# Kernel tuning notes

Measured on AMD Instinct MI355X. Metric: run time of the kernel, lower is better.

Reference implementation:

```python
import jax, jax.numpy as jnp
import numpy as np

C_CURV = 0.01   # manifold curvature c
EPS = 1e-7
KH = KW = 3
PAD = 1
STRIDE = 1


def log0(y):
    # Poincare-ball log map at origin: artanh(sqrt(c)||y||) * y / (sqrt(c)||y||)
    sqc = jnp.sqrt(jnp.asarray(C_CURV, y.dtype))
    n = jnp.maximum(jnp.linalg.norm(y, axis=-1, keepdims=True), EPS)
    return jnp.arctanh(jnp.clip(sqc * n, 0.0, 1.0 - 1e-6)) * y / (sqc * n)


def exp0(v):
    # Poincare-ball exp map at origin: tanh(sqrt(c)||v||) * v / (sqrt(c)||v||)
    sqc = jnp.sqrt(jnp.asarray(C_CURV, v.dtype))
    n = jnp.maximum(jnp.linalg.norm(v, axis=-1, keepdims=True), EPS)
    return jnp.tanh(sqc * n) * v / (sqc * n)


def setup_inputs() -> dict:
    key = jax.random.key(0)
    k1, k2, k3 = jax.random.split(key, 3)
    x = jax.random.uniform(k1, (4, 32, 256, 256), dtype=jnp.float32)  # points in ball (c=0.01 -> radius 10)
    Wk = jax.random.normal(k2, (KH * KW, 32, 32), dtype=jnp.float32) * 0.05  # [K, C_out, C_in]
    bias = jax.random.normal(k3, (32,), dtype=jnp.float32) * 0.01
    return {"x": x, "Wk": Wk, "bias": bias}


def reference(x, Wk, bias):
    B, Cin, H, W = x.shape
    Hout = (H + 2 * PAD - KH) // STRIDE + 1
    Wout = (W + 2 * PAD - KW) // STRIDE + 1
    xp = jnp.pad(x, ((0, 0), (0, 0), (PAD, PAD), (PAD, PAD)))
    # unfold: one slice per kernel position (i,j), matching F.unfold's (C_in, K, L) layout
    patches = jnp.stack(
        [xp[:, :, i:i + Hout * STRIDE:STRIDE, j:j + Wout * STRIDE:STRIDE]
         for i in range(KH) for j in range(KW)], axis=0)      # [K, B, Cin, Hout, Wout]
    u = log0(jnp.moveaxis(patches, 2, -1))                    # [K, B, Hout, Wout, Cin] tangent vectors
    # PVFC (mobius matvec = exp0(W @ log0(x))) followed by log0 cancels the exp0:
    # log0(PVFC_k(x)) = W_k @ log0(x). Aggregate (sum over k) fused into the einsum.
    v = jnp.einsum('kbhwc,koc->bhwo', u, Wk)                  # [B, Hout, Wout, Cout]
    v = jax.nn.relu(v + bias)
    out = exp0(v)                                             # back to manifold
    return jnp.transpose(out, (0, 3, 1, 2))                   # [B, Cout, Hout, Wout]
```

## Files before the change

### kernel.cpp

```cpp
#include <hip/hip_runtime.h>
#include <math.h>


#define TW 32
#define TH 8
#define HW_ 34
#define NPIX 340
#define CIN 32
#define COUT 32
#define U_BYTES 21760
#define W_ROWS 288

typedef __attribute__((ext_vector_type(8))) short bf16x8;
typedef __attribute__((ext_vector_type(4))) float f32x4;

__device__ inline unsigned short f2bf(float f) {
    unsigned int u = __builtin_bit_cast(unsigned int, f);
    unsigned int r = (u + 0x7FFFu + ((u >> 16) & 1u)) >> 16;
    return (unsigned short)r;
}

__global__ __launch_bounds__(256, 4) void pvconv_kernel(
    const float* __restrict__ x, const float* __restrict__ Wk,
    const float* __restrict__ bias, float* __restrict__ out)
{
    __shared__ __align__(16) unsigned char smem[U_BYTES + W_ROWS * 64];
    unsigned char* u8 = smem;
    unsigned char* w8 = smem + U_BYTES;
    float*         v  = (float*)smem;

    const int t  = threadIdx.x;
    const int bx = blockIdx.x, by = blockIdx.y, b = blockIdx.z;
    const int x0 = bx * TW, y0 = by * TH;

    for (int f = t; f < W_ROWS * 4; f += 256) {
        int r = f >> 2, j = f & 3;
        const float4* src = (const float4*)(Wk + r * 32 + j * 8);
        float4 a = src[0], c = src[1];
        unsigned int pk[4];
        pk[0] = (unsigned int)f2bf(a.x) | ((unsigned int)f2bf(a.y) << 16);
        pk[1] = (unsigned int)f2bf(a.z) | ((unsigned int)f2bf(a.w) << 16);
        pk[2] = (unsigned int)f2bf(c.x) | ((unsigned int)f2bf(c.y) << 16);
        pk[3] = (unsigned int)f2bf(c.z) | ((unsigned int)f2bf(c.w) << 16);
        int sw = j ^ ((r >> 1) & 3);
        *(uint4*)(w8 + r * 64 + sw * 16) = *(uint4*)pk;
    }

    for (int p = t; p < NPIX; p += 256) {
        int py = p / HW_, px = p - py * HW_;
        int gy = y0 - 1 + py, gx = x0 - 1 + px;
        float vv[CIN];
        if ((unsigned)gy < 256u && (unsigned)gx < 256u) {
            const float* xp = x + (size_t)b * CIN * 65536 + gy * 256 + gx;
            #pragma unroll
            for (int c = 0; c < CIN; ++c) vv[c] = xp[(size_t)c * 65536];
        } else {
            #pragma unroll
            for (int c = 0; c < CIN; ++c) vv[c] = 0.f;
        }
        float ss = 0.f;
        #pragma unroll
        for (int c = 0; c < CIN; ++c) ss = fmaf(vv[c], vv[c], ss);
        float n = fmaxf(sqrtf(ss), 1e-7f);
        float z = fminf(0.1f * n, 1.f - 1e-6f);
        float at = 0.5f * __logf((1.f + z) / (1.f - z));
        float s = at / (0.1f * n);
        int swb = (p >> 1) & 3;
        uint4* row = (uint4*)(u8 + p * 64);
        #pragma unroll
        for (int j = 0; j < 4; ++j) {
            unsigned int pk[4];
            #pragma unroll
            for (int w = 0; w < 4; ++w)
                pk[w] = (unsigned int)f2bf(vv[j * 8 + 2 * w] * s)
                      | ((unsigned int)f2bf(vv[j * 8 + 2 * w + 1] * s) << 16);
            row[j ^ swb] = *(uint4*)pk;
        }
    }
    __syncthreads();

    const int wv = t >> 6, lane = t & 63;
    const int m = lane & 15, quad = lane >> 4;

    f32x4 acc[2][4];
    #pragma unroll
    for (int n = 0; n < 2; ++n)
        #pragma unroll
        for (int mt = 0; mt < 4; ++mt) acc[n][mt] = (f32x4)0.f;

    int apix[4];
    #pragma unroll
    for (int mt = 0; mt < 4; ++mt) {
        int pb = wv * 64 + mt * 16;
        apix[mt] = (pb >> 5) * HW_ + (pb & 31) + m;
    }

    #pragma unroll
    for (int tap = 0; tap < 9; ++tap) {
        const int dy = tap / 3, dx = tap - dy * 3;
        const int hoff = dy * HW_ + dx;
        int r0 = tap * 32 + m;
        int swB = quad ^ ((r0 >> 1) & 3);
        bf16x8 bf0 = *(const bf16x8*)(w8 + r0 * 64 + swB * 16);
        bf16x8 bf1 = *(const bf16x8*)(w8 + (r0 + 16) * 64 + swB * 16);
        #pragma unroll
        for (int mt = 0; mt < 4; ++mt) {
            int hp = apix[mt] + hoff;
            bf16x8 af = *(const bf16x8*)(u8 + hp * 64 + ((quad ^ ((hp >> 1) & 3)) << 4));
            acc[0][mt] = __builtin_amdgcn_mfma_f32_16x16x32_bf16(af, bf0, acc[0][mt], 0, 0, 0);
            acc[1][mt] = __builtin_amdgcn_mfma_f32_16x16x32_bf16(af, bf1, acc[1][mt], 0, 0, 0);
        }
    }

    const float bia0 = bias[m], bia1 = bias[16 + m];
    __syncthreads();

    #pragma unroll
    for (int n = 0; n < 2; ++n)
        #pragma unroll
        for (int mt = 0; mt < 4; ++mt)
            #pragma unroll
            for (int r = 0; r < 4; ++r) {
                int pix = wv * 64 + mt * 16 + quad * 4 + r;
                float val = acc[n][mt][r] + (n ? bia1 : bia0);
                v[pix * 36 + n * 16 + m] = fmaxf(val, 0.f);
            }
    __syncthreads();

    {
        float q[COUT];
        const float4* vp = (const float4*)(smem + (size_t)t * 144);
        #pragma unroll
        for (int j = 0; j < 8; ++j) {
            float4 c4 = vp[j];
            q[4 * j] = c4.x; q[4 * j + 1] = c4.y; q[4 * j + 2] = c4.z; q[4 * j + 3] = c4.w;
        }
        float ss = 0.f;
        #pragma unroll
        for (int o = 0; o < COUT; ++o) ss = fmaf(q[o], q[o], ss);
        float n = fmaxf(sqrtf(ss), 1e-7f);
        float a = 0.1f * n;
        float e = __expf(-2.f * a);
        float s = (1.f - e) / ((1.f + e) * a);
        const int px = t & 31, py = t >> 5;
        const size_t base = (size_t)b * COUT * 65536 + (size_t)(y0 + py) * 256 + (x0 + px);
        #pragma unroll
        for (int o = 0; o < COUT; ++o)
            out[base + (size_t)o * 65536] = s * q[o];
    }
}

extern "C" void kernel_launch(void* const* d_in, const int* in_sizes, int n_in,
                              void* d_out, int out_size, void* d_ws, size_t ws_size,
                              hipStream_t stream) {
    const float* x    = (const float*)d_in[0];
    const float* Wk   = (const float*)d_in[1];
    const float* bias = (const float*)d_in[2];
    float* out = (float*)d_out;

    dim3 grid(256 / TW, 256 / TH, 4);
    dim3 block(256);
    pvconv_kernel<<<grid, block, 0, stream>>>(x, Wk, bias, out);
}
```

Before: 98.00 us.

## Prepack bf16 weights, vectorize halo loads, use 512-thread blocks with bf16 staging

```diff
diff --git a/kernel.cpp b/kernel.cpp
--- a/kernel.cpp
+++ b/kernel.cpp
@@ -8,145 +8,146 @@
 #define NPIX 340
 #define CIN 32
 #define COUT 32
-#define U_BYTES 21760
-#define W_ROWS 288
 
 typedef __attribute__((ext_vector_type(8))) short bf16x8;
 typedef __attribute__((ext_vector_type(4))) float f32x4;
 
 __device__ inline unsigned short f2bf(float f) {
     unsigned int u = __builtin_bit_cast(unsigned int, f);
-    unsigned int r = (u + 0x7FFFu + ((u >> 16) & 1u)) >> 16;
-    return (unsigned short)r;
+    return (unsigned short)((u + 0x7FFFu + ((u >> 16) & 1u)) >> 16);
+}
+__device__ inline unsigned int pk2(float a, float b) {
+    return (unsigned int)f2bf(a) | ((unsigned int)f2bf(b) << 16);
 }
 
-__global__ __launch_bounds__(256, 4) void pvconv_kernel(
-    const float* __restrict__ x, const float* __restrict__ Wk,
+__global__ __launch_bounds__(256) void wprep_kernel(
+    const float* __restrict__ Wk, unsigned short* __restrict__ wsW)
+{
+    int i = blockIdx.x * 256 + threadIdx.x;
+    if (i < 9 * 32 * 32) wsW[i] = f2bf(Wk[i]);
+}
+
+__global__ __launch_bounds__(512, 8) void pvconv_kernel(
+    const float* __restrict__ x, const unsigned short* __restrict__ wsW,
     const float* __restrict__ bias, float* __restrict__ out)
 {
-    __shared__ __align__(16) unsigned char smem[U_BYTES + W_ROWS * 64];
+    __shared__ __align__(16) unsigned char smem[NPIX * 64];
     unsigned char* u8 = smem;
-    unsigned char* w8 = smem + U_BYTES;
-    float*         v  = (float*)smem;
 
     const int t  = threadIdx.x;
-    const int bx = blockIdx.x, by = blockIdx.y, b = blockIdx.z;
-    const int x0 = bx * TW, y0 = by * TH;
+    const int x0 = blockIdx.x * TW, y0 = blockIdx.y * TH, b = blockIdx.z;
 
-    for (int f = t; f < W_ROWS * 4; f += 256) {
-        int r = f >> 2, j = f & 3;
-        const float4* src = (const float4*)(Wk + r * 32 + j * 8);
-        float4 a = src[0], c = src[1];
-        unsigned int pk[4];
-        pk[0] = (unsigned int)f2bf(a.x) | ((unsigned int)f2bf(a.y) << 16);
-        pk[1] = (unsigned int)f2bf(a.z) | ((unsigned int)f2bf(a.w) << 16);
-        pk[2] = (unsigned int)f2bf(c.x) | ((unsigned int)f2bf(c.y) << 16);
-        pk[3] = (unsigned int)f2bf(c.z) | ((unsigned int)f2bf(c.w) << 16);
-        int sw = j ^ ((r >> 1) & 3);
-        *(uint4*)(w8 + r * 64 + sw * 16) = *(uint4*)pk;
-    }
-
-    for (int p = t; p < NPIX; p += 256) {
-        int py = p / HW_, px = p - py * HW_;
-        int gy = y0 - 1 + py, gx = x0 - 1 + px;
-        float vv[CIN];
-        if ((unsigned)gy < 256u && (unsigned)gx < 256u) {
-            const float* xp = x + (size_t)b * CIN * 65536 + gy * 256 + gx;
+    if (t < 400) {
+        const int hy = t / 40, rem = t - hy * 40, j = rem >> 2, cq = rem & 3;
+        const int gy = y0 - 1 + hy;
+        const int gxb = x0 - 4 + 4 * j;
+        const bool ok = ((unsigned)gy < 256u) && !(j == 0 && x0 == 0)
+                                              && !(j == 9 && x0 == 224);
+        float vv[4][8];
+        if (ok) {
+            const float* xp = x + (size_t)(b * CIN + cq * 8) * 65536 + gy * 256 + gxb;
             #pragma unroll
-            for (int c = 0; c < CIN; ++c) vv[c] = xp[(size_t)c * 65536];
+            for (int cc = 0; cc < 8; ++cc) {
+                float4 f4 = *(const float4*)(xp + (size_t)cc * 65536);
+                vv[0][cc] = f4.x; vv[1][cc] = f4.y; vv[2][cc] = f4.z; vv[3][cc] = f4.w;
+            }
         } else {
             #pragma unroll
-            for (int c = 0; c < CIN; ++c) vv[c] = 0.f;
+            for (int i = 0; i < 4; ++i)
+                #pragma unroll
+                for (int cc = 0; cc < 8; ++cc) vv[i][cc] = 0.f;
         }
-        float ss = 0.f;
+        float s4[4];
         #pragma unroll
-        for (int c = 0; c < CIN; ++c) ss = fmaf(vv[c], vv[c], ss);
-        float n = fmaxf(sqrtf(ss), 1e-7f);
-        float z = fminf(0.1f * n, 1.f - 1e-6f);
-        float at = 0.5f * __logf((1.f + z) / (1.f - z));
-        float s = at / (0.1f * n);
-        int swb = (p >> 1) & 3;
-        uint4* row = (uint4*)(u8 + p * 64);
+        for (int i = 0; i < 4; ++i) {
+            float ss = 0.f;
+            #pragma unroll
+            for (int cc = 0; cc < 8; ++cc) ss = fmaf(vv[i][cc], vv[i][cc], ss);
+            ss += __shfl_xor(ss, 1);
+            ss += __shfl_xor(ss, 2);
+            float n = fmaxf(sqrtf(ss), 1e-7f);
+            float z = fminf(0.1f * n, 1.f - 1e-6f);
+            float at = 0.5f * __logf((1.f + z) / (1.f - z));
+            s4[i] = at / (0.1f * n);
+        }
+        const int i0 = (j == 0) ? 3 : 0, i1 = (j == 9) ? 0 : 3;
         #pragma unroll
-        for (int j = 0; j < 4; ++j) {
-            unsigned int pk[4];
+        for (int i = 0; i < 4; ++i) {
+            if (i < i0 || i > i1) continue;
+            int p = hy * 34 + 4 * j - 3 + i;
+            unsigned int pkk[4];
             #pragma unroll
             for (int w = 0; w < 4; ++w)
-                pk[w] = (unsigned int)f2bf(vv[j * 8 + 2 * w] * s)
-                      | ((unsigned int)f2bf(vv[j * 8 + 2 * w + 1] * s) << 16);
-            row[j ^ swb] = *(uint4*)pk;
+                pkk[w] = pk2(vv[i][2 * w] * s4[i], vv[i][2 * w + 1] * s4[i]);
+            *(uint4*)(u8 + p * 64 + ((cq ^ ((p >> 1) & 3)) << 4)) = *(uint4*)pkk;
         }
     }
     __syncthreads();
 
-    const int wv = t >> 6, lane = t & 63;
-    const int m = lane & 15, quad = lane >> 4;
+    const int wv = t >> 6, lane = t & 63, m = lane & 15, quad = lane >> 4;
+    const float bia0 = bias[m], bia1 = bias[16 + m];
 
-    f32x4 acc[2][4];
+    f32x4 acc[2][2];
     #pragma unroll
     for (int n = 0; n < 2; ++n)
         #pragma unroll
-        for (int mt = 0; mt < 4; ++mt) acc[n][mt] = (f32x4)0.f;
+        for (int mt = 0; mt < 2; ++mt) acc[n][mt] = (f32x4)0.f;
 
-    int apix[4];
-    #pragma unroll
-    for (int mt = 0; mt < 4; ++mt) {
-        int pb = wv * 64 + mt * 16;
-        apix[mt] = (pb >> 5) * HW_ + (pb & 31) + m;
-    }
-
+    const int pb0 = wv * 34 + m;
     #pragma unroll
     for (int tap = 0; tap < 9; ++tap) {
         const int dy = tap / 3, dx = tap - dy * 3;
-        const int hoff = dy * HW_ + dx;
-        int r0 = tap * 32 + m;
-        int swB = quad ^ ((r0 >> 1) & 3);
-        bf16x8 bf0 = *(const bf16x8*)(w8 + r0 * 64 + swB * 16);
-        bf16x8 bf1 = *(const bf16x8*)(w8 + (r0 + 16) * 64 + swB * 16);
+        const unsigned short* wrow = wsW + (tap * 32 + m) * 32 + quad * 8;
+        bf16x8 B0 = *(const bf16x8*)wrow;
+        bf16x8 B1 = *(const bf16x8*)(wrow + 512);
         #pragma unroll
-        for (int mt = 0; mt < 4; ++mt) {
-            int hp = apix[mt] + hoff;
-            bf16x8 af = *(const bf16x8*)(u8 + hp * 64 + ((quad ^ ((hp >> 1) & 3)) << 4));
-            acc[0][mt] = __builtin_amdgcn_mfma_f32_16x16x32_bf16(af, bf0, acc[0][mt], 0, 0, 0);
-            acc[1][mt] = __builtin_amdgcn_mfma_f32_16x16x32_bf16(af, bf1, acc[1][mt], 0, 0, 0);
+        for (int mt = 0; mt < 2; ++mt) {
+            int p = pb0 + mt * 16 + dy * 34 + dx;
+            bf16x8 A = *(const bf16x8*)(u8 + p * 64 + ((quad ^ ((p >> 1) & 3)) << 4));
+            acc[0][mt] = __builtin_amdgcn_mfma_f32_16x16x32_bf16(A, B0, acc[0][mt], 0, 0, 0);
+            acc[1][mt] = __builtin_amdgcn_mfma_f32_16x16x32_bf16(A, B1, acc[1][mt], 0, 0, 0);
         }
     }
-
-    const float bia0 = bias[m], bia1 = bias[16 + m];
     __syncthreads();
 
+    unsigned short* vb = (unsigned short*)smem;
     #pragma unroll
     for (int n = 0; n < 2; ++n)
         #pragma unroll
-        for (int mt = 0; mt < 4; ++mt)
+        for (int mt = 0; mt < 2; ++mt)
             #pragma unroll
             for (int r = 0; r < 4; ++r) {
-                int pix = wv * 64 + mt * 16 + quad * 4 + r;
+                int P = wv * 32 + mt * 16 + quad * 4 + r;
                 float val = acc[n][mt][r] + (n ? bia1 : bia0);
-                v[pix * 36 + n * 16 + m] = fmaxf(val, 0.f);
+                vb[P * 40 + n * 16 + m] = f2bf(fmaxf(val, 0.f));
             }
     __syncthreads();
 
     {
-        float q[COUT];
-        const float4* vp = (const float4*)(smem + (size_t)t * 144);
+        const int pix = t >> 1, h = t & 1;
+        const unsigned short* vp = (const unsigned short*)smem + pix * 40 + h * 16;
+        uint4 q0 = *(const uint4*)vp;
+        uint4 q1 = *(const uint4*)(vp + 8);
+        unsigned int wds[8] = {q0.x, q0.y, q0.z, q0.w, q1.x, q1.y, q1.z, q1.w};
+        float qf[16];
         #pragma unroll
-        for (int j = 0; j < 8; ++j) {
-            float4 c4 = vp[j];
-            q[4 * j] = c4.x; q[4 * j + 1] = c4.y; q[4 * j + 2] = c4.z; q[4 * j + 3] = c4.w;
+        for (int k = 0; k < 8; ++k) {
+            qf[2 * k]     = __builtin_bit_cast(float, wds[k] << 16);
+            qf[2 * k + 1] = __builtin_bit_cast(float, wds[k] & 0xFFFF0000u);
         }
         float ss = 0.f;
         #pragma unroll
-        for (int o = 0; o < COUT; ++o) ss = fmaf(q[o], q[o], ss);
+        for (int k = 0; k < 16; ++k) ss = fmaf(qf[k], qf[k], ss);
+        ss += __shfl_xor(ss, 1);
         float n = fmaxf(sqrtf(ss), 1e-7f);
         float a = 0.1f * n;
         float e = __expf(-2.f * a);
         float s = (1.f - e) / ((1.f + e) * a);
-        const int px = t & 31, py = t >> 5;
+        const int py = pix >> 5, px = pix & 31;
         const size_t base = (size_t)b * COUT * 65536 + (size_t)(y0 + py) * 256 + (x0 + px);
         #pragma unroll
-        for (int o = 0; o < COUT; ++o)
-            out[base + (size_t)o * 65536] = s * q[o];
+        for (int cc = 0; cc < 16; ++cc)
+            out[base + (size_t)(h * 16 + cc) * 65536] = s * qf[cc];
     }
 }
 
@@ -157,8 +158,9 @@
     const float* Wk   = (const float*)d_in[1];
     const float* bias = (const float*)d_in[2];
     float* out = (float*)d_out;
+    unsigned short* wsW = (unsigned short*)d_ws;
 
+    wprep_kernel<<<dim3(36), dim3(256), 0, stream>>>(Wk, wsW);
     dim3 grid(256 / TW, 256 / TH, 4);
-    dim3 block(256);
-    pvconv_kernel<<<grid, block, 0, stream>>>(x, Wk, bias, out);
+    pvconv_kernel<<<grid, dim3(512), 0, stream>>>(x, wsW, bias, out);
 }
```

Result: slower. 101.4 us (+3.5%).
